# Optimization experiments

Measured on AMD Instinct MI355X. Metric: run time of the kernel, lower is better.

Reference implementation:

```python
import jax, jax.numpy as jnp
import numpy as np

N = 64
DX0 = np.pi / N
B = 4096
N_ENV = 8
CODE = 128


def setup_inputs() -> dict:
    key = jax.random.key(0)
    k1, k2, k3 = jax.random.split(key, 3)
    y0 = jax.random.normal(k1, (B, 1, N, N), dtype=jnp.float32)
    env = jax.random.randint(k2, (B,), 0, N_ENV).astype(jnp.int64)
    codes = jax.random.normal(k3, (B, CODE), dtype=jnp.float32)
    t = jnp.zeros((1,), dtype=jnp.float32)
    # learned params: [mu, domain_placeholder] per env (matches nn.Parameter init)
    params = jnp.concatenate([jnp.full((N_ENV, 1), 0.005, jnp.float32),
                              jnp.full((N_ENV, 1), 1.0, jnp.float32)], axis=1)
    # fixed domain buffer for n_env == 8
    domain = jnp.array([0.75, 1.0, 0.75, 1.0, 0.75, 1.0, 0.75, 1.0],
                       dtype=jnp.float32)[:, None]  # [n_env, 1]
    return {"t": t, "y0": y0, "env": env, "codes": codes,
            "params": params, "domain": domain}


def _dx(a):  # roll along last axis (torch dims=2 on [B,H,W])
    return jnp.roll(a, -1, axis=2) - jnp.roll(a, 1, axis=2)


def _dy(a):  # roll along axis 1
    return jnp.roll(a, -1, axis=1) - jnp.roll(a, 1, axis=1)


def _laplacian2d(a, fdx2):
    # torch conv2d (cross-correlation) with kernel [[0,1,0],[1,-4,1],[1,1,0]]
    # and circular padding; note the asymmetric bottom row (faithful to source).
    lap = (jnp.roll(a, 1, axis=1)                    # a[i-1, j]
           + jnp.roll(a, 1, axis=2)                  # a[i, j-1]
           - 4.0 * a
           + jnp.roll(a, -1, axis=2)                 # a[i, j+1]
           + jnp.roll(jnp.roll(a, -1, axis=1), 1, axis=2)  # a[i+1, j-1]
           + jnp.roll(a, -1, axis=1))                # a[i+1, j]
    return lap / fdx2


def _poisson_solve(w, fdx):
    # w: [B,N,N]; fdx: [B,1] grid spacing per sample
    w_pad = jnp.pad(w, ((0, 0), (0, 1), (0, 1)), mode='wrap')  # [B,N+1,N+1]
    wf = jnp.fft.fft2(w_pad / (N ** 2))
    base = jnp.fft.fftfreq(N + 1).astype(w.dtype)       # fftfreq(n, d) = base / d
    k = (2.0 * np.pi) * base[None, :] / fdx             # [B, N+1]
    k2 = k[:, :, None] ** 2 + k[:, None, :] ** 2        # [B, N+1, N+1]
    uf = -wf / (1e-12 + k2)
    uf = uf.at[:, 0, 0].set(0.0)
    return jnp.fft.ifft2((N ** 2) * uf).real[:, :N, :N]


def reference(t, y0, env, codes, params, domain):
    x = y0[:, 0]                              # [B,N,N]
    p = params[env]                           # [B,2]
    mu = p[:, 0:1][..., None]                 # [B,1,1]
    fdx = domain[env] * DX0                   # [B,1]
    psi = _poisson_solve(-x, fdx)             # [B,N,N]
    fdx2 = (fdx[..., None]) ** 2              # [B,1,1]

    rxm = jnp.roll(x, -1, axis=2); rxp = jnp.roll(x, 1, axis=2)
    rym = jnp.roll(x, -1, axis=1); ryp = jnp.roll(x, 1, axis=1)
    pxm = jnp.roll(psi, -1, axis=2); pxp = jnp.roll(psi, 1, axis=2)
    pym = jnp.roll(psi, -1, axis=1); pyp = jnp.roll(psi, 1, axis=1)

    J1 = (_dy(psi) * _dx(x) - _dx(psi) * _dy(x)) / (4.0 * fdx2)
    J2 = (rxm * _dy(pxm) - rxp * _dy(pxp)
          - rym * _dx(pym) + ryp * _dx(pyp)) / (4.0 * fdx2)
    J3 = (jnp.roll(rxm, -1, axis=1) * (pym - pxm)
          - jnp.roll(rxp, 1, axis=1) * (pxp - pyp)
          - jnp.roll(rxp, -1, axis=1) * (pym - pxp)
          + jnp.roll(rxm, 1, axis=1) * (pxm - pyp)) / (4.0 * fdx2)

    dudt = -(J1 + J2 + J3) / 3.0 + mu * _laplacian2d(x, fdx2)
    return dudt[:, None]                      # [B,1,N,N]
```

## Files before the change

### kernel.cpp

```cpp
#include <hip/hip_runtime.h>
#include <math.h>


typedef _Float16 half8 __attribute__((ext_vector_type(8)));
typedef _Float16 half4 __attribute__((ext_vector_type(4)));
typedef float floatx4 __attribute__((ext_vector_type(4)));

#define WPI 0.09666439165562847f

#define H_TB1 0
#define H_TA2 10240
#define H_TG  20480
#define H_TH  26624
#define F_GR32 16384
#define F_GI32 16432
#define F_HC32 16480
#define F_HS32 16528
#define F_SE   16576
#define F_SEG  (F_SE + 264)

#define ARENA 40448
#define NB 4
#define OFF_YT   0
#define OFF_XR   0
#define OFF_XI   9216
#define OFF_X32R 18432
#define OFF_X32I 18688
#define OFF_ST   18944
#define OFF_S32  37952
#define OFF_PSIT 18944

__device__ __forceinline__ float trig65(int t, int isSin) {
    return isSin ? __sinf(WPI * (float)t) : __cosf(WPI * (float)t);
}

__global__ void setup_tables(float* __restrict__ ws, const float* __restrict__ domain) {
    int idx = blockIdx.x * 256 + threadIdx.x;
    _Float16* tbH = (_Float16*)ws;
    const float inv = 1.0f / 4225.0f;
    if (idx < 32768) {
        float v = 0.0f;
        int part;
        if (idx < 10240) {
            int chunk = idx >> 9, within = idx & 511;
            part = chunk & 1; int kc = (chunk >> 1) & 1, ni = chunk >> 2;
            int l2 = within >> 3, j = within & 7;
            int row = 16 * ni + (l2 & 15);
            int k = 32 * kc + 8 * (l2 >> 4) + j;
            if (row < 66) {
                int c = (row < 32) ? row : (row < 64 ? row - 32 : 32);
                int isS = (row < 32) ? 0 : (row < 64 ? 1 : row - 64);
                v = trig65((k * c) % 65, isS);
                if (k == 0) v += trig65((64 * c) % 65, isS);
            }
        } else if (idx < 20480) {
            int i2 = idx - 10240;
            int chunk = i2 >> 9, within = i2 & 511;
            part = chunk & 1; int kc = (chunk >> 1) & 1, mi = chunk >> 2;
            int l2 = within >> 3, j = within & 7;
            int row = 16 * mi + (l2 & 15);
            int m = 32 * kc + 8 * (l2 >> 4) + j;
            if (row < 66) {
                int jr = (row < 32) ? row : (row < 64 ? row - 32 : 32);
                int isS = (row < 32) ? 0 : (row < 64 ? 1 : row - 64);
                float s = isS ? 1.0f : -1.0f;
                v = s * trig65((jr * m) % 65, isS);
                if (m == 0) v += s * trig65((jr * 64) % 65, isS);
            }
        } else if (idx < 26624) {
            int i2 = idx - 20480;
            int chunk = i2 >> 9, within = i2 & 511;
            part = chunk & 1; int g = (chunk >> 1) & 1, si = chunk >> 2;
            int l2 = within >> 3, j = within & 7;
            int s = 16 * si + (l2 & 15);
            int jj = 8 * (l2 >> 4) + j;
            if (s <= 32) v = trig65((s * jj) % 65, g);
        } else {
            int i2 = idx - 26624;
            int chunk = i2 >> 9, within = i2 & 511;
            part = chunk & 1; int h = (chunk >> 1) & 1, pi2 = chunk >> 2;
            int l2 = within >> 3, j = within & 7;
            int p = 16 * pi2 + (l2 & 15);
            int c = 8 * (l2 >> 4) + j;
            if (p <= 32) {
                if (c == 0) v = h ? 0.0f : inv;
                else v = 2.0f * inv * trig65((c * p) % 65, h);
            }
        }
        _Float16 hh = (_Float16)v;
        tbH[idx] = part ? (_Float16)(v - (float)hh) : hh;
    } else if (idx < 32960) {
        int i2 = idx - 32768;
        int grp = i2 / 48, s = i2 - grp * 48;
        float v = 0.0f;
        if (s <= 32) {
            int t = (32 * s) % 65;
            float cs = __cosf(WPI * t), sn = __sinf(WPI * t);
            v = (grp == 0) ? cs : (grp == 1) ? sn : (grp == 2) ? 2.0f * inv * cs : 2.0f * inv * sn;
        }
        ws[F_GR32 + i2] = v;
    } else if (idx < 41672) {
        int i2 = idx - 32960;
        const float DX0 = 0.04908738521234052f;
        int e2, a, b2;
        if (i2 < 264) { e2 = i2 / 33; a = i2 - e2 * 33; b2 = 32; }
        else {
            int i3 = i2 - 264;
            e2 = i3 / 1056;
            int rem = i3 - e2 * 1056;
            a = rem >> 5; b2 = rem & 31;
        }
        float fdx = domain[e2] * DX0;
        float tt = 6.283185307179586f / (65.0f * fdx);
        float s2v = tt * tt;
        ws[F_SE + i2] = -1.0f / (1e-12f + s2v * (float)(a * a + b2 * b2));
    }
}

#define MFMA16(A, B, C) __builtin_amdgcn_mfma_f32_16x16x32_f16((A), (B), (C), 0, 0, 0)

__global__ __launch_bounds__(512, 2)
void turb_kernel(const float* __restrict__ y0, const int* __restrict__ env,
                 const float* __restrict__ params, const float* __restrict__ domain,
                 const float* __restrict__ ws, float* __restrict__ out) {
    __shared__ __align__(16) char lds_raw[NB * ARENA];

    const int b0 = blockIdx.x * NB, tid = threadIdx.x;
    const int wid = __builtin_amdgcn_readfirstlane(tid >> 6);
    const int lane = tid & 63, n16 = lane & 15, q = lane >> 4;
    const int lane8 = lane * 8;
    const _Float16* tbH = (const _Float16*)ws;
    const float* tf = ws;

    int eA[NB];
    const float *SegA[NB], *Se3A[NB], *xA[NB];
    float* outA[NB];
    float invfA[NB], inv12A[NB];
    const float DX0 = 0.04908738521234052f;
    #pragma unroll
    for (int t = 0; t < NB; t++) {
        eA[t] = __builtin_amdgcn_readfirstlane(env[b0 + t]);
        SegA[t] = tf + F_SEG + eA[t] * 1056;
        Se3A[t] = tf + F_SE + eA[t] * 33;
        xA[t]   = y0 + (size_t)(b0 + t) * 4096;
        outA[t] = out + (size_t)(b0 + t) * 4096;
        float mu = params[2 * eA[t]];
        float f = domain[eA[t]] * DX0, f2 = f * f;
        inv12A[t] = 1.0f / (12.0f * f2);
        invfA[t] = mu / f2;
    }

    {
        const int mi = wid & 3;
        half8 Ah[NB][2], Al[NB][2];
        #pragma unroll
        for (int t = 0; t < NB; t++) {
            const float* xrow = xA[t] + (16 * mi + n16) * 64 + 8 * q;
            #pragma unroll
            for (int kc = 0; kc < 2; kc++) {
                float4 v0 = *(const float4*)(xrow + 32 * kc);
                float4 v1 = *(const float4*)(xrow + 32 * kc + 4);
                float vv[8] = {v0.x, v0.y, v0.z, v0.w, v1.x, v1.y, v1.z, v1.w};
                #pragma unroll
                for (int u = 0; u < 8; u++) {
                    _Float16 h = (_Float16)vv[u];
                    Ah[t][kc][u] = h; Al[t][kc][u] = (_Float16)(vv[u] - (float)h);
                }
            }
        }
        const int niBeg = (wid & 4) ? 3 : 0;
        const int niEnd = (wid & 4) ? 5 : 3;
        for (int ni = niBeg; ni < niEnd; ni++) {
            const _Float16* tb = tbH + H_TB1 + ni * 2048 + lane8;
            half8 B0h = *(const half8*)(tb);
            half8 B0l = *(const half8*)(tb + 512);
            half8 B1h = *(const half8*)(tb + 1024);
            half8 B1l = *(const half8*)(tb + 1536);
            const int cp = 16 * ni + n16;
            const bool st = (ni < 4 || n16 < 2);
            #pragma unroll
            for (int t = 0; t < NB; t++) {
                floatx4 acc = {0.f, 0.f, 0.f, 0.f};
                acc = MFMA16(Ah[t][0], B0h, acc); acc = MFMA16(Ah[t][0], B0l, acc); acc = MFMA16(Al[t][0], B0h, acc);
                acc = MFMA16(Ah[t][1], B1h, acc); acc = MFMA16(Ah[t][1], B1l, acc); acc = MFMA16(Al[t][1], B1h, acc);
                if (st) {
                    half4 hh, ll;
                    #pragma unroll
                    for (int i = 0; i < 4; i++) {
                        _Float16 h = (_Float16)acc[i];
                        hh[i] = h; ll[i] = (_Float16)(acc[i] - (float)h);
                    }
                    _Float16* Yt = (_Float16*)(lds_raw + t * ARENA + OFF_YT);
                    *(half4*)(Yt + cp * 136 + 16 * mi + 4 * q) = hh;
                    *(half4*)(Yt + cp * 136 + 64 + 16 * mi + 4 * q) = ll;
                }
            }
        }
    }
    __syncthreads();

    {
        int pos = wid;
        half8 Ah0, Al0, Ah1, Al1;
        {
            const _Float16* ta = tbH + H_TA2 + (pos / 5) * 2048 + lane8;
            Ah0 = *(const half8*)(ta);
            Al0 = *(const half8*)(ta + 512);
            Ah1 = *(const half8*)(ta + 1024);
            Al1 = *(const half8*)(ta + 1536);
        }
        while (pos < 25) {
            const int mi = pos / 5, ni = pos - 5 * mi;
            const int npos = pos + 8;
            half8 nAh0 = {}, nAl0 = {}, nAh1 = {}, nAl1 = {};
            if (npos < 25) {
                const _Float16* ta = tbH + H_TA2 + (npos / 5) * 2048 + lane8;
                nAh0 = *(const half8*)(ta);
                nAl0 = *(const half8*)(ta + 512);
                nAh1 = *(const half8*)(ta + 1024);
                nAl1 = *(const half8*)(ta + 1536);
            }
            const int yoff = (16 * ni + n16) * 136 + 8 * q;
            const int cp = 16 * ni + n16;
            const int cc = (ni == 4) ? 32 : (cp & 31);
            const int isS = (ni == 4) ? n16 : (ni >> 1);
            const bool valid = (ni < 4) || (n16 < 2);
            #pragma unroll
            for (int t = 0; t < NB; t++) {
                const _Float16* Yt = (const _Float16*)(lds_raw + t * ARENA + OFF_YT);
                const _Float16* yrow = Yt + yoff;
                half8 Bh0 = *(const half8*)(yrow);
                half8 Bl0 = *(const half8*)(yrow + 64);
                half8 Bh1 = *(const half8*)(yrow + 32);
                half8 Bl1 = *(const half8*)(yrow + 96);
                floatx4 acc = {0.f, 0.f, 0.f, 0.f};
                acc = MFMA16(Ah0, Bh0, acc); acc = MFMA16(Ah0, Bl0, acc); acc = MFMA16(Al0, Bh0, acc);
                acc = MFMA16(Ah1, Bh1, acc); acc = MFMA16(Ah1, Bl1, acc); acc = MFMA16(Al1, Bh1, acc);
                if (valid) {
                    _Float16* ST = (_Float16*)(lds_raw + t * ARENA + OFF_ST);
                    float* S32 = (float*)(lds_raw + t * ARENA + OFF_S32);
                    if (mi < 4) {
                        const int isQ = mi >> 1;
                        const int sid = isQ ? (isS ? 3 : 1) : (isS ? 2 : 0);
                        const int jjb = 16 * (mi & 1) + 4 * q;
                        floatx4 Sv = *(const floatx4*)(SegA[t] + cc * 32 + jjb);
                        float ssg = (sid == 2) ? -2.0f : 2.0f;
                        half4 hh, ll;
                        #pragma unroll
                        for (int i = 0; i < 4; i++) {
                            float v = ssg * Sv[i] * acc[i];
                            _Float16 h = (_Float16)v;
                            hh[i] = h; ll[i] = (_Float16)(v - (float)h);
                        }
                        _Float16* sb = ST + sid * 2376 + cc * 72 + jjb;
                        *(half4*)sb = hh;
                        *(half4*)(sb + 32) = ll;
                    } else if (q == 0) {
                        float S = Se3A[t][cc];
                        #pragma unroll
                        for (int i = 0; i < 2; i++) {
                            int sid = i ? (isS ? 3 : 1) : (isS ? 2 : 0);
                            float v = 2.0f * S * acc[i];
                            if (sid == 2) v = -v;
                            S32[sid * 36 + cc] = v;
                        }
                    }
                }
            }
            Ah0 = nAh0; Al0 = nAl0; Ah1 = nAh1; Al1 = nAl1;
            pos = npos;
        }
    }
    __syncthreads();

    if (wid < NB && lane < 33) {
        _Float16* ST = (_Float16*)(lds_raw + wid * ARENA + OFF_ST);
        const int c = lane;
        float v0[4];
        #pragma unroll
        for (int sid = 0; sid < 4; sid++)
            v0[sid] = (float)ST[sid * 2376 + c * 72] + (float)ST[sid * 2376 + c * 72 + 32];
        float pr = 0.5f * (v0[0] + v0[3]), pi = 0.5f * (v0[1] + v0[2]);
        if (c == 0) { pr = 0.f; pi = 0.f; }
        float outs[4] = {pr, pi, pi, pr};
        #pragma unroll
        for (int sid = 0; sid < 4; sid++) {
            _Float16 h = (_Float16)outs[sid];
            ST[sid * 2376 + c * 72] = h;
            ST[sid * 2376 + c * 72 + 32] = (_Float16)(outs[sid] - (float)h);
        }
    }
    __syncthreads();

    for (int pos = wid; pos < 18; pos += 8) {
        const int ci = pos / 6, rem = pos - 6 * ci;
        const int si = rem >> 1, g = rem & 1;
        const _Float16* tg = tbH + H_TG + si * 2048 + lane8;
        half8 Grh = *(const half8*)(tg);
        half8 Grl = *(const half8*)(tg + 512);
        half8 Gih = *(const half8*)(tg + 1024);
        half8 Gil = *(const half8*)(tg + 1536);
        const int s = 16 * si + n16;
        const float ga = tf[F_GR32 + s], gi2 = tf[F_GI32 + s];
        const bool sval = (si < 2) || (n16 == 0);
        const float sgn = g ? 1.0f : -1.0f;
        const int cb = 16 * ci + 4 * q;
        const int aoff = (2 * g) * 2376 + (16 * ci + n16) * 72 + 8 * q;
        #pragma unroll
        for (int t = 0; t < NB; t++) {
            const _Float16* ST = (const _Float16*)(lds_raw + t * ARENA + OFF_ST);
            const float* S32 = (const float*)(lds_raw + t * ARENA + OFF_S32);
            const _Float16* st0 = ST + aoff;
            half8 A0h = *(const half8*)(st0),        A0l = *(const half8*)(st0 + 32);
            half8 A1h = *(const half8*)(st0 + 2376), A1l = *(const half8*)(st0 + 2376 + 32);
            floatx4 aA = {0.f,0.f,0.f,0.f}, aB = aA;
            aA = MFMA16(A0h, Grh, aA); aA = MFMA16(A0h, Grl, aA); aA = MFMA16(A0l, Grh, aA);
            aB = MFMA16(A1h, Gih, aB); aB = MFMA16(A1h, Gil, aB); aB = MFMA16(A1l, Gih, aB);
            _Float16* Xo = (_Float16*)(lds_raw + t * ARENA + (g ? OFF_XI : OFF_XR));
            float* X32o = (float*)(lds_raw + t * ARENA + (g ? OFF_X32I : OFF_X32R));
            if (ci < 2) {
                floatx4 U0 = *(const floatx4*)(S32 + (2 * g) * 36 + cb);
                floatx4 U1 = *(const floatx4*)(S32 + (2 * g + 1) * 36 + cb);
                half4 hP, lP, hM, lM;
                #pragma unroll
                for (int i = 0; i < 4; i++) {
                    float av = aA[i] + ga * U0[i], bv = aB[i] + gi2 * U1[i];
                    float xP = av + sgn * bv;
                    float xM = av - sgn * bv;
                    _Float16 h;
                    h = (_Float16)xP; hP[i] = h; lP[i] = (_Float16)(xP - (float)h);
                    h = (_Float16)xM; hM[i] = h; lM[i] = (_Float16)(xM - (float)h);
                }
                if (sval) {
                    *(half4*)(Xo + s * 72 + cb) = hP;  *(half4*)(Xo + s * 72 + 32 + cb) = lP;
                    if (s >= 2) {
                        int sm = 65 - s;
                        *(half4*)(Xo + sm * 72 + cb) = hM;  *(half4*)(Xo + sm * 72 + 32 + cb) = lM;
                    }
                }
            } else if (q == 0 && sval) {
                float u0 = S32[(2 * g) * 36 + 32], u1 = S32[(2 * g + 1) * 36 + 32];
                float av = aA[0] + ga * u0, bv = aB[0] + gi2 * u1;
                X32o[s] = av + sgn * bv;
                if (s >= 2) X32o[65 - s] = av - sgn * bv;
            }
        }
    }
    __syncthreads();

    for (int p48 = wid; p48 < 48; p48 += 8) {
        const int t = p48 / 12;
        const int pos = p48 - 12 * t;
        const int ri = pos / 3, pti = pos - 3 * ri;
        const char* base = lds_raw + t * ARENA;
        const _Float16* Xr = (const _Float16*)(base + OFF_XR);
        const _Float16* Xi = (const _Float16*)(base + OFF_XI);
        const float* X32r = (const float*)(base + OFF_X32R);
        const float* X32i = (const float*)(base + OFF_X32I);
        float* psiT = (float*)(base + OFF_PSIT);
        const int brow = (16 * ri + n16) * 72 + 8 * q;
        half8 Brh = *(const half8*)(Xr + brow), Brl = *(const half8*)(Xr + brow + 32);
        half8 Bih = *(const half8*)(Xi + brow), Bil = *(const half8*)(Xi + brow + 32);
        const _Float16* th = tbH + H_TH + pti * 2048 + lane8;
        half8 Hch = *(const half8*)(th);
        half8 Hcl = *(const half8*)(th + 512);
        half8 Hsh = *(const half8*)(th + 1024);
        half8 Hsl = *(const half8*)(th + 1536);
        floatx4 aE = {0.f,0.f,0.f,0.f}, aF = aE;
        aE = MFMA16(Hch, Brh, aE); aE = MFMA16(Hch, Brl, aE); aE = MFMA16(Hcl, Brh, aE);
        aF = MFMA16(Hsh, Bih, aF); aF = MFMA16(Hsh, Bil, aF); aF = MFMA16(Hsl, Bih, aF);
        const int r = 16 * ri + n16;
        float xr32 = X32r[r], xi32 = X32i[r];
        if (pti < 2) {
            const int pb = 16 * pti + 4 * q;
            floatx4 Hc4 = *(const floatx4*)(tf + F_HC32 + pb);
            floatx4 Hs4 = *(const floatx4*)(tf + F_HS32 + pb);
            float* pp = psiT + pb * 65 + r;
            float* pm = psiT + (65 - pb) * 65 + r;
            #pragma unroll
            for (int i = 0; i < 4; i++) {
                float E = aE[i] + xr32 * Hc4[i];
                float F = aF[i] + xi32 * Hs4[i];
                pp[i * 65] = E - F;
                if (pb + i >= 2) pm[-i * 65] = E + F;
            }
        } else if (q == 0) {
            float E = aE[0] + xr32 * tf[F_HC32 + 32];
            float F = aF[0] + xi32 * tf[F_HS32 + 32];
            psiT[32 * 65 + r] = E - F;
            psiT[33 * 65 + r] = E + F;
        }
    }
    __syncthreads();

    #pragma unroll
    for (int t = 0; t < NB; t++) {
        const float* psiT = (const float*)(lds_raw + t * ARENA + OFF_PSIT);
        const float* x0 = xA[t];
        const float inv12 = inv12A[t], invf = invfA[t];
        const int c = lane;
        const int cm1 = (c + 63) & 63, cp1 = (c + 1) & 63;
        const int r0 = wid * 8;
        const float* xL = x0 + r0 * 64 + cm1;
        const float* xC = x0 + r0 * 64 + c;
        const float* xR = x0 + r0 * 64 + cp1;
        const float* pL = psiT + cm1 * 65 + r0;
        const float* pC = psiT + c * 65 + r0;
        const float* pR = psiT + cp1 * 65 + r0;
        float* ob = outA[t] + r0 * 64 + c;
        const int mo = (wid == 0) ? 63 : -1;
        float xLm = xL[mo * 64], xCm = xC[mo * 64], xRm = xR[mo * 64];
        float pLm = pL[mo], pCm = pC[mo], pRm = pR[mo];
        float xLc = xL[0], xCc = xC[0], xRc = xR[0];
        float pLc = pL[0], pCc = pC[0], pRc = pR[0];
        #pragma unroll
        for (int it = 0; it < 8; it++) {
            int ro = it + 1;
            if (it == 7 && wid == 7) ro = -56;
            float xLp = xL[ro * 64], xCp = xC[ro * 64], xRp = xR[ro * 64];
            float pLp = pL[ro], pCp = pC[ro], pRp = pR[ro];
            float J1 = (pCp - pCm) * (xRc - xLc) - (pRc - pLc) * (xCp - xCm);
            float J2 = xRc * (pRp - pRm) - xLc * (pLp - pLm) - xCp * (pRp - pLp) + xCm * (pRm - pLm);
            float J3 = xRp * (pCp - pRc) - xLm * (pLc - pCm) - xLp * (pCp - pLc) + xRm * (pRc - pCm);
            float lap = xCm + xLc - 4.f * xCc + xRc + xLp + xCp;
            ob[it * 64] = -(J1 + J2 + J3) * inv12 + lap * invf;
            xLm = xLc; xCm = xCc; xRm = xRc; pLm = pLc; pCm = pCc; pRm = pRc;
            xLc = xLp; xCc = xCp; xRc = xRp; pLc = pLp; pCc = pCp; pRc = pRp;
        }
    }
}

extern "C" void kernel_launch(void* const* d_in, const int* in_sizes, int n_in,
                              void* d_out, int out_size, void* d_ws, size_t ws_size,
                              hipStream_t stream) {
    const float* y0     = (const float*)d_in[1];
    const int*   env    = (const int*)d_in[2];
    const float* params = (const float*)d_in[4];
    const float* domain = (const float*)d_in[5];
    float* out = (float*)d_out;
    float* ws  = (float*)d_ws;

    setup_tables<<<dim3(163), dim3(256), 0, stream>>>(ws, domain);
    turb_kernel<<<dim3(1024), dim3(512), 0, stream>>>(y0, env, params, domain, ws, out);
}
```

Baseline: 198.9 us.

## Halve samples per block and double waves to 16 per block

Each block now handles 2 samples instead of 4 and runs 1024 threads (16 waves), so the grid doubles to 2048 blocks. Work distribution in every stage is remapped to 16 waves: the first DFT stage splits column tiles per wave group, and the stencil stage gives each wave 4 rows instead of 8. The software prefetch of twiddle tables in the second stage is dropped in favour of direct loads. This trades fewer samples amortising table loads per block for more parallel waves, smaller LDS per block and more blocks resident; the launch bound of 1024 threads with 4 blocks may force tight register limits.

```diff
diff --git a/kernel.cpp b/kernel.cpp
--- a/kernel.cpp
+++ b/kernel.cpp
@@ -20,7 +20,7 @@
 #define F_SEG  (F_SE + 264)
 
 #define ARENA 40448
-#define NB 4
+#define NB 2
 #define OFF_YT   0
 #define OFF_XR   0
 #define OFF_XI   9216
@@ -119,7 +119,7 @@
 
 #define MFMA16(A, B, C) __builtin_amdgcn_mfma_f32_16x16x32_f16((A), (B), (C), 0, 0, 0)
 
-__global__ __launch_bounds__(512, 2)
+__global__ __launch_bounds__(1024, 4)
 void turb_kernel(const float* __restrict__ y0, const int* __restrict__ env,
                  const float* __restrict__ params, const float* __restrict__ domain,
                  const float* __restrict__ ws, float* __restrict__ out) {
@@ -152,6 +152,7 @@
 
     {
         const int mi = wid & 3;
+        const int g1 = wid >> 2;
         half8 Ah[NB][2], Al[NB][2];
         #pragma unroll
         for (int t = 0; t < NB; t++) {
@@ -168,8 +169,8 @@
                 }
             }
         }
-        const int niBeg = (wid & 4) ? 3 : 0;
-        const int niEnd = (wid & 4) ? 5 : 3;
+        const int niBeg = (g1 == 0) ? 0 : g1 + 1;
+        const int niEnd = (g1 == 0) ? 2 : g1 + 2;
         for (int ni = niBeg; ni < niEnd; ni++) {
             const _Float16* tb = tbH + H_TB1 + ni * 2048 + lane8;
             half8 B0h = *(const half8*)(tb);
@@ -199,76 +200,59 @@
     }
     __syncthreads();
 
-    {
-        int pos = wid;
-        half8 Ah0, Al0, Ah1, Al1;
-        {
-            const _Float16* ta = tbH + H_TA2 + (pos / 5) * 2048 + lane8;
-            Ah0 = *(const half8*)(ta);
-            Al0 = *(const half8*)(ta + 512);
-            Ah1 = *(const half8*)(ta + 1024);
-            Al1 = *(const half8*)(ta + 1536);
-        }
-        while (pos < 25) {
-            const int mi = pos / 5, ni = pos - 5 * mi;
-            const int npos = pos + 8;
-            half8 nAh0 = {}, nAl0 = {}, nAh1 = {}, nAl1 = {};
-            if (npos < 25) {
-                const _Float16* ta = tbH + H_TA2 + (npos / 5) * 2048 + lane8;
-                nAh0 = *(const half8*)(ta);
-                nAl0 = *(const half8*)(ta + 512);
-                nAh1 = *(const half8*)(ta + 1024);
-                nAl1 = *(const half8*)(ta + 1536);
-            }
-            const int yoff = (16 * ni + n16) * 136 + 8 * q;
-            const int cp = 16 * ni + n16;
-            const int cc = (ni == 4) ? 32 : (cp & 31);
-            const int isS = (ni == 4) ? n16 : (ni >> 1);
-            const bool valid = (ni < 4) || (n16 < 2);
-            #pragma unroll
-            for (int t = 0; t < NB; t++) {
-                const _Float16* Yt = (const _Float16*)(lds_raw + t * ARENA + OFF_YT);
-                const _Float16* yrow = Yt + yoff;
-                half8 Bh0 = *(const half8*)(yrow);
-                half8 Bl0 = *(const half8*)(yrow + 64);
-                half8 Bh1 = *(const half8*)(yrow + 32);
-                half8 Bl1 = *(const half8*)(yrow + 96);
-                floatx4 acc = {0.f, 0.f, 0.f, 0.f};
-                acc = MFMA16(Ah0, Bh0, acc); acc = MFMA16(Ah0, Bl0, acc); acc = MFMA16(Al0, Bh0, acc);
-                acc = MFMA16(Ah1, Bh1, acc); acc = MFMA16(Ah1, Bl1, acc); acc = MFMA16(Al1, Bh1, acc);
-                if (valid) {
-                    _Float16* ST = (_Float16*)(lds_raw + t * ARENA + OFF_ST);
-                    float* S32 = (float*)(lds_raw + t * ARENA + OFF_S32);
-                    if (mi < 4) {
-                        const int isQ = mi >> 1;
-                        const int sid = isQ ? (isS ? 3 : 1) : (isS ? 2 : 0);
-                        const int jjb = 16 * (mi & 1) + 4 * q;
-                        floatx4 Sv = *(const floatx4*)(SegA[t] + cc * 32 + jjb);
-                        float ssg = (sid == 2) ? -2.0f : 2.0f;
-                        half4 hh, ll;
-                        #pragma unroll
-                        for (int i = 0; i < 4; i++) {
-                            float v = ssg * Sv[i] * acc[i];
-                            _Float16 h = (_Float16)v;
-                            hh[i] = h; ll[i] = (_Float16)(v - (float)h);
-                        }
-                        _Float16* sb = ST + sid * 2376 + cc * 72 + jjb;
-                        *(half4*)sb = hh;
-                        *(half4*)(sb + 32) = ll;
-                    } else if (q == 0) {
-                        float S = Se3A[t][cc];
-                        #pragma unroll
-                        for (int i = 0; i < 2; i++) {
-                            int sid = i ? (isS ? 3 : 1) : (isS ? 2 : 0);
-                            float v = 2.0f * S * acc[i];
-                            if (sid == 2) v = -v;
-                            S32[sid * 36 + cc] = v;
-                        }
+    for (int pos = wid; pos < 25; pos += 16) {
+        const int mi = pos / 5, ni = pos - 5 * mi;
+        const _Float16* ta = tbH + H_TA2 + mi * 2048 + lane8;
+        half8 Ah0 = *(const half8*)(ta);
+        half8 Al0 = *(const half8*)(ta + 512);
+        half8 Ah1 = *(const half8*)(ta + 1024);
+        half8 Al1 = *(const half8*)(ta + 1536);
+        const int yoff = (16 * ni + n16) * 136 + 8 * q;
+        const int cp = 16 * ni + n16;
+        const int cc = (ni == 4) ? 32 : (cp & 31);
+        const int isS = (ni == 4) ? n16 : (ni >> 1);
+        const bool valid = (ni < 4) || (n16 < 2);
+        #pragma unroll
+        for (int t = 0; t < NB; t++) {
+            const _Float16* Yt = (const _Float16*)(lds_raw + t * ARENA + OFF_YT);
+            const _Float16* yrow = Yt + yoff;
+            half8 Bh0 = *(const half8*)(yrow);
+            half8 Bl0 = *(const half8*)(yrow + 64);
+            half8 Bh1 = *(const half8*)(yrow + 32);
+            half8 Bl1 = *(const half8*)(yrow + 96);
+            floatx4 acc = {0.f, 0.f, 0.f, 0.f};
+            acc = MFMA16(Ah0, Bh0, acc); acc = MFMA16(Ah0, Bl0, acc); acc = MFMA16(Al0, Bh0, acc);
+            acc = MFMA16(Ah1, Bh1, acc); acc = MFMA16(Ah1, Bl1, acc); acc = MFMA16(Al1, Bh1, acc);
+            if (valid) {
+                _Float16* ST = (_Float16*)(lds_raw + t * ARENA + OFF_ST);
+                float* S32 = (float*)(lds_raw + t * ARENA + OFF_S32);
+                if (mi < 4) {
+                    const int isQ = mi >> 1;
+                    const int sid = isQ ? (isS ? 3 : 1) : (isS ? 2 : 0);
+                    const int jjb = 16 * (mi & 1) + 4 * q;
+                    floatx4 Sv = *(const floatx4*)(SegA[t] + cc * 32 + jjb);
+                    float ssg = (sid == 2) ? -2.0f : 2.0f;
+                    half4 hh, ll;
+                    #pragma unroll
+                    for (int i = 0; i < 4; i++) {
+                        float v = ssg * Sv[i] * acc[i];
+                        _Float16 h = (_Float16)v;
+                        hh[i] = h; ll[i] = (_Float16)(v - (float)h);
+                    }
+                    _Float16* sb = ST + sid * 2376 + cc * 72 + jjb;
+                    *(half4*)sb = hh;
+                    *(half4*)(sb + 32) = ll;
+                } else if (q == 0) {
+                    float S = Se3A[t][cc];
+                    #pragma unroll
+                    for (int i = 0; i < 2; i++) {
+                        int sid = i ? (isS ? 3 : 1) : (isS ? 2 : 0);
+                        float v = 2.0f * S * acc[i];
+                        if (sid == 2) v = -v;
+                        S32[sid * 36 + cc] = v;
                     }
                 }
             }
-            Ah0 = nAh0; Al0 = nAl0; Ah1 = nAh1; Al1 = nAl1;
-            pos = npos;
         }
     }
     __syncthreads();
@@ -292,7 +276,7 @@
     }
     __syncthreads();
 
-    for (int pos = wid; pos < 18; pos += 8) {
+    for (int pos = wid; pos < 18; pos += 16) {
         const int ci = pos / 6, rem = pos - 6 * ci;
         const int si = rem >> 1, g = rem & 1;
         const _Float16* tg = tbH + H_TG + si * 2048 + lane8;
@@ -348,9 +332,9 @@
     }
     __syncthreads();
 
-    for (int p48 = wid; p48 < 48; p48 += 8) {
-        const int t = p48 / 12;
-        const int pos = p48 - 12 * t;
+    for (int p24 = wid; p24 < 24; p24 += 16) {
+        const int t = p24 / 12;
+        const int pos = p24 - 12 * t;
         const int ri = pos / 3, pti = pos - 3 * ri;
         const char* base = lds_raw + t * ARENA;
         const _Float16* Xr = (const _Float16*)(base + OFF_XR);
@@ -400,7 +384,7 @@
         const float inv12 = inv12A[t], invf = invfA[t];
         const int c = lane;
         const int cm1 = (c + 63) & 63, cp1 = (c + 1) & 63;
-        const int r0 = wid * 8;
+        const int r0 = wid * 4;
         const float* xL = x0 + r0 * 64 + cm1;
         const float* xC = x0 + r0 * 64 + c;
         const float* xR = x0 + r0 * 64 + cp1;
@@ -414,9 +398,9 @@
         float xLc = xL[0], xCc = xC[0], xRc = xR[0];
         float pLc = pL[0], pCc = pC[0], pRc = pR[0];
         #pragma unroll
-        for (int it = 0; it < 8; it++) {
+        for (int it = 0; it < 4; it++) {
             int ro = it + 1;
-            if (it == 7 && wid == 7) ro = -56;
+            if (it == 3 && wid == 15) ro = -60;
             float xLp = xL[ro * 64], xCp = xC[ro * 64], xRp = xR[ro * 64];
             float pLp = pL[ro], pCp = pC[ro], pRp = pR[ro];
             float J1 = (pCp - pCm) * (xRc - xLc) - (pRc - pLc) * (xCp - xCm);
@@ -441,5 +425,5 @@
     float* ws  = (float*)d_ws;
 
     setup_tables<<<dim3(163), dim3(256), 0, stream>>>(ws, domain);
-    turb_kernel<<<dim3(1024), dim3(512), 0, stream>>>(y0, env, params, domain, ws, out);
+    turb_kernel<<<dim3(2048), dim3(1024), 0, stream>>>(y0, env, params, domain, ws, out);
 }
```

New measurement: 203.4 us. 1.02x slower.
